# Kernel optimization log

Hardware: AMD Instinct MI355X
Metric: run time of the kernel (lower is better)

Reference implementation:

```python
import jax, jax.numpy as jnp
import numpy as np

NUM_NODES = 10000  # nodes per graph
TOTAL_NODES = 80000  # nbatches (8) * NUM_NODES
N_EDGES = 2560000
IN_DIM, H1, H2 = 128, 32, 64


def setup_inputs() -> dict:
    key = jax.random.key(0)
    ks = jax.random.split(key, 8)
    x = jax.random.normal(ks[0], (TOTAL_NODES, IN_DIM), dtype=jnp.float32)
    ei = jax.random.randint(ks[1], (2, N_EDGES), 0, TOTAL_NODES, dtype=jnp.int64)
    # GCNConv weights (PyG convention: x @ W then propagate, bias after aggregation)
    W1 = jax.random.normal(ks[2], (IN_DIM, H1), dtype=jnp.float32) / np.sqrt(IN_DIM)
    b1 = jax.random.normal(ks[3], (H1,), dtype=jnp.float32) * 0.01
    W2 = jax.random.normal(ks[4], (H1, H2), dtype=jnp.float32) / np.sqrt(H1)
    b2 = jax.random.normal(ks[5], (H2,), dtype=jnp.float32) * 0.01
    Wout = jax.random.normal(ks[6], (H2 * NUM_NODES, 1), dtype=jnp.float32) / np.sqrt(H2 * NUM_NODES)
    bout = jax.random.normal(ks[7], (1,), dtype=jnp.float32) * 0.01
    return {"x": x, "ei": ei, "W1": W1, "b1": b1, "W2": W2, "b2": b2, "Wout": Wout, "bout": bout}


def reference(x, ei, W1, b1, W2, b2, Wout, bout):
    N = x.shape[0]
    # PyG GCNConv: add self-loops, symmetric normalization D^-1/2 (A+I) D^-1/2
    loop = jnp.arange(N, dtype=ei.dtype)
    src = jnp.concatenate([ei[0], loop])
    dst = jnp.concatenate([ei[1], loop])
    deg = jax.ops.segment_sum(jnp.ones_like(src, dtype=x.dtype), dst, num_segments=N)
    dinv = jnp.where(deg > 0, jax.lax.rsqrt(deg), 0.0)
    norm = (dinv[src] * dinv[dst])[:, None]  # [E+N, 1]

    def gcn(h, W, b):
        h = h @ W                     # linear transform first (small feature dim)
        msg = h[src] * norm           # gather + scale
        agg = jax.ops.segment_sum(msg, dst, num_segments=N)  # scatter-add
        return agg + b

    h = jax.nn.relu(gcn(x, W1, b1))
    h = jax.nn.relu(gcn(h, W2, b2))
    nbatches = N // NUM_NODES
    flat = h.reshape(nbatches, NUM_NODES * h.shape[1])
    return flat @ Wout + bout  # [nbatches, 1]
```

## Files before the change

### kernel.cpp

```cpp
#include <hip/hip_runtime.h>
#include <hip/hip_fp16.h>

constexpr int   N_NODES = 80000;
constexpr int   N_EDGE  = 2560000;
constexpr int   IN_DIM  = 128;
constexpr int   H1      = 32;
constexpr int   H2      = 64;
constexpr int   NPB     = 10000;
constexpr int   NB      = 8;
constexpr int   G2_BLOCKS = N_NODES / 8;
constexpr int   BLK_PER_BATCH = G2_BLOCKS / NB;

constexpr int   BKT_SHIFT = 8;
constexpr int   BKT_N     = 1 << BKT_SHIFT;
constexpr int   NBKT      = (N_NODES + BKT_N - 1) >> BKT_SHIFT;
constexpr int   BBSTRIDE  = 16;
constexpr unsigned SBKT_CAP = 9216;
constexpr int   BF_EPB    = 4096;
constexpr int   BF_BLOCKS = N_EDGE / BF_EPB;
constexpr int   BF_THREADS = 512;
constexpr int   BF_EPT    = BF_EPB / BF_THREADS;

constexpr int   G1_ROWS   = 64;
constexpr int   G1_BLOCKS = N_NODES / G1_ROWS;

__global__ void k_initb(unsigned* __restrict__ bbump) {
    int i = blockIdx.x * blockDim.x + threadIdx.x;
    if (i < NBKT) bbump[i * BBSTRIDE] = (unsigned)i * SBKT_CAP;
}

__global__ __launch_bounds__(BF_THREADS) void k_binfill(
        const int* __restrict__ ei, unsigned* __restrict__ bbump,
        unsigned* __restrict__ stage) {
    __shared__ unsigned hist[NBKT];
    __shared__ unsigned base[NBKT];
    int t = threadIdx.x;
    int e0 = blockIdx.x * BF_EPB;
    for (int i = t; i < NBKT; i += BF_THREADS) hist[i] = 0u;
    __syncthreads();
    unsigned dcache[BF_EPT];
#pragma unroll
    for (int k = 0; k < BF_EPT; ++k) {
        unsigned d = (unsigned)ei[N_EDGE + e0 + t + k * BF_THREADS];
        dcache[k] = d;
        atomicAdd(&hist[d >> BKT_SHIFT], 1u);
    }
    __syncthreads();
    for (int i = t; i < NBKT; i += BF_THREADS) {
        unsigned h = hist[i];
        base[i] = h ? atomicAdd(&bbump[i * BBSTRIDE], h) : 0u;
        hist[i] = 0u;
    }
    __syncthreads();
#pragma unroll
    for (int k = 0; k < BF_EPT; ++k) {
        int s = ei[e0 + t + k * BF_THREADS];
        unsigned d = dcache[k];
        int bkt = (int)(d >> BKT_SHIFT);
        unsigned lp = atomicAdd(&hist[bkt], 1u);
        unsigned pos = base[bkt] + lp;
        if (pos < (unsigned)(bkt + 1) * SBKT_CAP)
            stage[pos] = ((unsigned)s << BKT_SHIFT) | (d & (BKT_N - 1u));
    }
}

__global__ __launch_bounds__(256) void k_place(
        const unsigned* __restrict__ bbump, const unsigned* __restrict__ stage,
        int* __restrict__ csr, unsigned* __restrict__ row_ptr,
        unsigned* __restrict__ rend, float* __restrict__ dinv) {
    __shared__ unsigned cnt[BKT_N];
    __shared__ unsigned sc[BKT_N];
    __shared__ unsigned nb[BKT_N];
    int b = blockIdx.x;
    int t = threadIdx.x;
    unsigned beg = (unsigned)b * SBKT_CAP;
    unsigned end = min(bbump[b * BBSTRIDE], (unsigned)(b + 1) * SBKT_CAP);
    cnt[t] = 0u;
    __syncthreads();
    for (unsigned j = beg + (unsigned)t; j < end; j += 256)
        atomicAdd(&cnt[stage[j] & (BKT_N - 1u)], 1u);
    __syncthreads();
    sc[t] = cnt[t];
    for (int ofs = 1; ofs < BKT_N; ofs <<= 1) {
        __syncthreads();
        unsigned u = (t >= ofs) ? sc[t - ofs] : 0u;
        __syncthreads();
        sc[t] += u;
    }
    __syncthreads();
    {
        unsigned nodebase = beg + sc[t] - cnt[t];
        int node = (b << BKT_SHIFT) + t;
        if (node < N_NODES) {
            row_ptr[node] = nodebase;
            rend[node]    = nodebase + cnt[t];
            dinv[node] = rsqrtf((float)(cnt[t] + 1u));
        }
        nb[t] = nodebase;
    }
    __syncthreads();
    for (unsigned j = beg + (unsigned)t; j < end; j += 256) {
        unsigned v = stage[j];
        unsigned pos = atomicAdd(&nb[v & (BKT_N - 1u)], 1u);
        csr[pos] = (int)(v >> BKT_SHIFT);
    }
}

__global__ __launch_bounds__(256) void k_gemm1(
        const float* __restrict__ x, const float* __restrict__ W1,
        const float* __restrict__ dinv, __half* __restrict__ xW1h) {
    __shared__ float W1s[IN_DIM * H1];
    __shared__ float xs[G1_ROWS * IN_DIM];
    int tid = threadIdx.x;
    for (int i = tid; i < IN_DIM * H1; i += 256) W1s[i] = W1[i];
    int row0 = blockIdx.x * G1_ROWS;
    const float4* src4 = reinterpret_cast<const float4*>(x + (size_t)row0 * IN_DIM);
    float4* xs4 = reinterpret_cast<float4*>(xs);
#pragma unroll
    for (int k = 0; k < 8; ++k) xs4[tid + k * 256] = src4[tid + k * 256];
    __syncthreads();
    int c = tid & 31, g = tid >> 5;
    float acc[8] = {0.f, 0.f, 0.f, 0.f, 0.f, 0.f, 0.f, 0.f};
    for (int j = 0; j < IN_DIM / 4; ++j) {
        float w0 = W1s[(4 * j + 0) * H1 + c];
        float w1 = W1s[(4 * j + 1) * H1 + c];
        float w2 = W1s[(4 * j + 2) * H1 + c];
        float w3 = W1s[(4 * j + 3) * H1 + c];
#pragma unroll
        for (int r = 0; r < 8; ++r) {
            float4 a = *reinterpret_cast<const float4*>(&xs[((g * 8 + r) << 7) + 4 * j]);
            acc[r] += a.x * w0 + a.y * w1 + a.z * w2 + a.w * w3;
        }
    }
#pragma unroll
    for (int r = 0; r < 8; ++r) {
        int row = row0 + g * 8 + r;
        xW1h[(size_t)row * H1 + c] = __float2half(acc[r] * dinv[row]);
    }
}

__global__ __launch_bounds__(256) void k_gather1_gemm2(
        const unsigned* __restrict__ row_ptr, const unsigned* __restrict__ rend,
        const int* __restrict__ csr, const __half* __restrict__ xW1h,
        const float* __restrict__ dinv, const float* __restrict__ b1,
        const float* __restrict__ W2, __half* __restrict__ h2h) {
    int wave = threadIdx.x >> 6;
    int lane = threadIdx.x & 63;
    int h = lane >> 5;
    int q = (lane >> 2) & 7;
    int t = lane & 3;
    int d = blockIdx.x * 8 + wave * 2 + h;
    unsigned beg = row_ptr[d], end = rend[d];
    float acc[8] = {0.f, 0.f, 0.f, 0.f, 0.f, 0.f, 0.f, 0.f};
    const __half2 one2  = __float2half2_rn(1.0f);
    const __half2 zero2 = __float2half2_rn(0.0f);
    for (unsigned base = beg; base < end; base += 32) {
        __half2 hacc[4] = {zero2, zero2, zero2, zero2};
#pragma unroll
        for (int it = 0; it < 2; ++it) {
            unsigned j0 = base + (unsigned)(it * 16) + (unsigned)q;
            unsigned j1 = j0 + 8u;
            int     s0 = (j0 < end) ? csr[j0] : 0;
            __half2 m0 = (j0 < end) ? one2 : zero2;
            int     s1 = (j1 < end) ? csr[j1] : 0;
            __half2 m1 = (j1 < end) ? one2 : zero2;
            float4 raw0 = *reinterpret_cast<const float4*>(xW1h + (size_t)s0 * H1 + 8 * t);
            float4 raw1 = *reinterpret_cast<const float4*>(xW1h + (size_t)s1 * H1 + 8 * t);
            const __half2* h0 = reinterpret_cast<const __half2*>(&raw0);
            const __half2* h1 = reinterpret_cast<const __half2*>(&raw1);
#pragma unroll
            for (int i = 0; i < 4; ++i) {
                hacc[i] = __hfma2(h0[i], m0, hacc[i]);
                hacc[i] = __hfma2(h1[i], m1, hacc[i]);
            }
        }
#pragma unroll
        for (int i = 0; i < 4; ++i) {
            float2 f = __half22float2(hacc[i]);
            acc[2 * i]     += f.x;
            acc[2 * i + 1] += f.y;
        }
    }
#pragma unroll
    for (int m = 4; m <= 16; m <<= 1)
#pragma unroll
        for (int i = 0; i < 8; ++i)
            acc[i] += __shfl_xor(acc[i], m, 64);
    float dv = dinv[d];
    float4 sraw = *reinterpret_cast<const float4*>(xW1h + (size_t)d * H1 + 8 * t);
    const __half2* sh = reinterpret_cast<const __half2*>(&sraw);
    float rel[8];
#pragma unroll
    for (int i = 0; i < 4; ++i) {
        float2 f = __half22float2(sh[i]);
        rel[2 * i]     = fmaxf((acc[2 * i]     + f.x) * dv + b1[8 * t + 2 * i],     0.f);
        rel[2 * i + 1] = fmaxf((acc[2 * i + 1] + f.y) * dv + b1[8 * t + 2 * i + 1], 0.f);
    }
    int c = lane & 31;
    float h2a = 0.f, h2b = 0.f;
#pragma unroll
    for (int k = 0; k < H1; ++k) {
        int src = (lane & 32) | (k >> 3);
        float r = __shfl(rel[k & 7], src, 64);
        h2a += r * W2[k * H2 + c];
        h2b += r * W2[k * H2 + c + 32];
    }
    h2h[(size_t)d * H2 + c]      = __float2half(h2a * dv);
    h2h[(size_t)d * H2 + c + 32] = __float2half(h2b * dv);
}

__global__ __launch_bounds__(256) void k_gather2_final(
        const unsigned* __restrict__ row_ptr, const unsigned* __restrict__ rend,
        const int* __restrict__ csr, const __half* __restrict__ h2h,
        const float* __restrict__ dinv, const float* __restrict__ b2,
        const float* __restrict__ Wout, double* __restrict__ partial2) {
    int wave = threadIdx.x >> 6;
    int lane = threadIdx.x & 63;
    int h = lane >> 5;
    int o = (lane >> 3) & 3;
    int t = lane & 7;
    int d = blockIdx.x * 8 + wave * 2 + h;
    unsigned beg = row_ptr[d], end = rend[d];
    float acc[8] = {0.f, 0.f, 0.f, 0.f, 0.f, 0.f, 0.f, 0.f};
    const __half2 one2  = __float2half2_rn(1.0f);
    const __half2 zero2 = __float2half2_rn(0.0f);
    for (unsigned base = beg; base < end; base += 16) {
        __half2 hacc[4] = {zero2, zero2, zero2, zero2};
#pragma unroll
        for (int it = 0; it < 2; ++it) {
            unsigned j0 = base + (unsigned)(it * 8) + (unsigned)o;
            unsigned j1 = j0 + 4u;
            int     s0 = (j0 < end) ? csr[j0] : 0;
            __half2 m0 = (j0 < end) ? one2 : zero2;
            int     s1 = (j1 < end) ? csr[j1] : 0;
            __half2 m1 = (j1 < end) ? one2 : zero2;
            float4 raw0 = *reinterpret_cast<const float4*>(h2h + (size_t)s0 * H2 + 8 * t);
            float4 raw1 = *reinterpret_cast<const float4*>(h2h + (size_t)s1 * H2 + 8 * t);
            const __half2* h0 = reinterpret_cast<const __half2*>(&raw0);
            const __half2* h1 = reinterpret_cast<const __half2*>(&raw1);
#pragma unroll
            for (int i = 0; i < 4; ++i) {
                hacc[i] = __hfma2(h0[i], m0, hacc[i]);
                hacc[i] = __hfma2(h1[i], m1, hacc[i]);
            }
        }
#pragma unroll
        for (int i = 0; i < 4; ++i) {
            float2 f = __half22float2(hacc[i]);
            acc[2 * i]     += f.x;
            acc[2 * i + 1] += f.y;
        }
    }
#pragma unroll
    for (int m = 8; m <= 16; m <<= 1)
#pragma unroll
        for (int i = 0; i < 8; ++i)
            acc[i] += __shfl_xor(acc[i], m, 64);
    float dv = dinv[d];
    float4 sraw = *reinterpret_cast<const float4*>(h2h + (size_t)d * H2 + 8 * t);
    const __half2* sh = reinterpret_cast<const __half2*>(&sraw);
    float4 bb0 = *reinterpret_cast<const float4*>(b2 + 8 * t);
    float4 bb1 = *reinterpret_cast<const float4*>(b2 + 8 * t + 4);
    const float* wrow = Wout + (size_t)(d % NPB) * H2 + 8 * t;
    float4 ww0 = *reinterpret_cast<const float4*>(wrow);
    float4 ww1 = *reinterpret_cast<const float4*>(wrow + 4);
    float self[8];
#pragma unroll
    for (int i = 0; i < 4; ++i) {
        float2 f = __half22float2(sh[i]);
        self[2 * i] = f.x; self[2 * i + 1] = f.y;
    }
    float bbv[8] = {bb0.x, bb0.y, bb0.z, bb0.w, bb1.x, bb1.y, bb1.z, bb1.w};
    float wwv[8] = {ww0.x, ww0.y, ww0.z, ww0.w, ww1.x, ww1.y, ww1.z, ww1.w};
    float fsum = 0.f;
#pragma unroll
    for (int i = 0; i < 8; ++i)
        fsum += fmaxf((acc[i] + self[i]) * dv + bbv[i], 0.f) * wwv[i];
    double dval = (double)fsum;
    dval += __shfl_down(dval, 4, 64);
    dval += __shfl_down(dval, 2, 64);
    dval += __shfl_down(dval, 1, 64);
    __shared__ double sdbl[8];
    if ((lane & 31) == 0) sdbl[wave * 2 + h] = dval;
    __syncthreads();
    if (threadIdx.x == 0)
        partial2[blockIdx.x] = ((sdbl[0] + sdbl[1]) + (sdbl[2] + sdbl[3]))
                             + ((sdbl[4] + sdbl[5]) + (sdbl[6] + sdbl[7]));
}

__global__ __launch_bounds__(256) void k_reduce(
        const double* __restrict__ partial2, const float* __restrict__ bout,
        float* __restrict__ out) {
    int b = blockIdx.x;
    int tid = threadIdx.x;
    double acc = 0.0;
    for (int i = tid; i < BLK_PER_BATCH; i += 256)
        acc += partial2[b * BLK_PER_BATCH + i];
    for (int off = 32; off; off >>= 1) acc += __shfl_down(acc, off, 64);
    __shared__ double sred[4];
    if ((tid & 63) == 0) sred[tid >> 6] = acc;
    __syncthreads();
    if (tid == 0)
        out[b] = (float)(((sred[0] + sred[1]) + (sred[2] + sred[3])) + (double)bout[0]);
}

extern "C" void kernel_launch(void* const* d_in, const int* in_sizes, int n_in,
                              void* d_out, int out_size, void* d_ws, size_t ws_size,
                              hipStream_t stream) {
    const float* x    = (const float*)d_in[0];
    const int*   ei   = (const int*)d_in[1];
    const float* W1   = (const float*)d_in[2];
    const float* b1   = (const float*)d_in[3];
    const float* W2   = (const float*)d_in[4];
    const float* b2   = (const float*)d_in[5];
    const float* Wout = (const float*)d_in[6];
    const float* bout = (const float*)d_in[7];
    float* out = (float*)d_out;

    constexpr size_t STATIC_SZ = (size_t)NBKT * SBKT_CAP;
    char* ws = (char*)d_ws;
    size_t off = 0;
    int*      csr     = (int*)(ws + off);      off += STATIC_SZ * 4;
    unsigned* stage   = (unsigned*)(ws + off); off += STATIC_SZ * 4;
    __half*   xW1h    = (__half*)(ws + off);   off += (size_t)N_NODES * H1 * 2;
    __half*   h2h     = (__half*)(ws + off);   off += (size_t)N_NODES * H2 * 2;
    unsigned* row_ptr = (unsigned*)(ws + off); off += (size_t)N_NODES * 4;
    unsigned* rend    = (unsigned*)(ws + off); off += (size_t)N_NODES * 4;
    float*    dinv    = (float*)(ws + off);    off += (size_t)N_NODES * 4;
    unsigned* bbump   = (unsigned*)(ws + off); off += (size_t)NBKT * BBSTRIDE * 4;
    double*   partial2= (double*)(ws + off);   off += (size_t)G2_BLOCKS * 8;
    (void)ws_size; (void)in_sizes; (void)n_in; (void)out_size;

    const int B = 256;
    k_initb<<<(NBKT + B - 1) / B, B, 0, stream>>>(bbump);
    k_binfill<<<BF_BLOCKS, BF_THREADS, 0, stream>>>(ei, bbump, stage);
    k_place<<<NBKT, B, 0, stream>>>(bbump, stage, csr, row_ptr, rend, dinv);

    k_gemm1<<<G1_BLOCKS, B, 0, stream>>>(x, W1, dinv, xW1h);
    k_gather1_gemm2<<<N_NODES / 8, B, 0, stream>>>(row_ptr, rend, csr, xW1h, dinv, b1, W2, h2h);
    k_gather2_final<<<G2_BLOCKS, B, 0, stream>>>(row_ptr, rend, csr, h2h, dinv, b2, Wout, partial2);

    k_reduce<<<NB, B, 0, stream>>>(partial2, bout, out);
}
```

Measured before the change: 175.0 us.

## Merge GEMM1 into edge binning launch and apply dinv scaling in place

The first-layer GEMM no longer depends on dinv, so it now runs as extra blocks of the edge-binning kernel. This overlaps the compute-heavy GEMM with the atomic-heavy binning and saves one launch. The per-node dinv scaling of xW1 moves into k_place, which rescales its bucket's fp16 rows in place. The cost is an extra read-modify-write pass over xW1h and a second fp16 rounding. The fused kernel also uses a 48KB static shared buffer, which can lower occupancy for the binning blocks.

```diff
diff --git a/kernel.cpp b/kernel.cpp
--- a/kernel.cpp
+++ b/kernel.cpp
@@ -18,59 +18,96 @@
 constexpr unsigned SBKT_CAP = 9216;
 constexpr int   BF_EPB    = 4096;
 constexpr int   BF_BLOCKS = N_EDGE / BF_EPB;
-constexpr int   BF_THREADS = 512;
-constexpr int   BF_EPT    = BF_EPB / BF_THREADS;
+constexpr int   FB_THREADS = 512;
+constexpr int   BF_EPT    = BF_EPB / FB_THREADS;
 
 constexpr int   G1_ROWS   = 64;
 constexpr int   G1_BLOCKS = N_NODES / G1_ROWS;
+constexpr int   FUSED_BLOCKS = BF_BLOCKS + G1_BLOCKS;
 
 __global__ void k_initb(unsigned* __restrict__ bbump) {
     int i = blockIdx.x * blockDim.x + threadIdx.x;
     if (i < NBKT) bbump[i * BBSTRIDE] = (unsigned)i * SBKT_CAP;
 }
 
-__global__ __launch_bounds__(BF_THREADS) void k_binfill(
+__global__ __launch_bounds__(FB_THREADS) void k_binfill_gemm1(
         const int* __restrict__ ei, unsigned* __restrict__ bbump,
-        unsigned* __restrict__ stage) {
-    __shared__ unsigned hist[NBKT];
-    __shared__ unsigned base[NBKT];
+        unsigned* __restrict__ stage,
+        const float* __restrict__ x, const float* __restrict__ W1,
+        __half* __restrict__ xW1h) {
+    __shared__ __align__(16) char smem[49152];
     int t = threadIdx.x;
-    int e0 = blockIdx.x * BF_EPB;
-    for (int i = t; i < NBKT; i += BF_THREADS) hist[i] = 0u;
-    __syncthreads();
-    unsigned dcache[BF_EPT];
-#pragma unroll
-    for (int k = 0; k < BF_EPT; ++k) {
-        unsigned d = (unsigned)ei[N_EDGE + e0 + t + k * BF_THREADS];
-        dcache[k] = d;
-        atomicAdd(&hist[d >> BKT_SHIFT], 1u);
-    }
-    __syncthreads();
-    for (int i = t; i < NBKT; i += BF_THREADS) {
-        unsigned h = hist[i];
-        base[i] = h ? atomicAdd(&bbump[i * BBSTRIDE], h) : 0u;
-        hist[i] = 0u;
-    }
-    __syncthreads();
-#pragma unroll
-    for (int k = 0; k < BF_EPT; ++k) {
-        int s = ei[e0 + t + k * BF_THREADS];
-        unsigned d = dcache[k];
-        int bkt = (int)(d >> BKT_SHIFT);
-        unsigned lp = atomicAdd(&hist[bkt], 1u);
-        unsigned pos = base[bkt] + lp;
-        if (pos < (unsigned)(bkt + 1) * SBKT_CAP)
-            stage[pos] = ((unsigned)s << BKT_SHIFT) | (d & (BKT_N - 1u));
+    if (blockIdx.x < BF_BLOCKS) {
+        unsigned* hist = (unsigned*)smem;
+        unsigned* base = hist + NBKT;
+        int e0 = blockIdx.x * BF_EPB;
+        for (int i = t; i < NBKT; i += FB_THREADS) hist[i] = 0u;
+        __syncthreads();
+        unsigned dcache[BF_EPT];
+#pragma unroll
+        for (int k = 0; k < BF_EPT; ++k) {
+            unsigned d = (unsigned)ei[N_EDGE + e0 + t + k * FB_THREADS];
+            dcache[k] = d;
+            atomicAdd(&hist[d >> BKT_SHIFT], 1u);
+        }
+        __syncthreads();
+        for (int i = t; i < NBKT; i += FB_THREADS) {
+            unsigned h = hist[i];
+            base[i] = h ? atomicAdd(&bbump[i * BBSTRIDE], h) : 0u;
+            hist[i] = 0u;
+        }
+        __syncthreads();
+#pragma unroll
+        for (int k = 0; k < BF_EPT; ++k) {
+            int s = ei[e0 + t + k * FB_THREADS];
+            unsigned d = dcache[k];
+            int bkt = (int)(d >> BKT_SHIFT);
+            unsigned lp = atomicAdd(&hist[bkt], 1u);
+            unsigned pos = base[bkt] + lp;
+            if (pos < (unsigned)(bkt + 1) * SBKT_CAP)
+                stage[pos] = ((unsigned)s << BKT_SHIFT) | (d & (BKT_N - 1u));
+        }
+    } else {
+        float* W1s = (float*)smem;
+        float* xs  = W1s + IN_DIM * H1;
+        int bb = blockIdx.x - BF_BLOCKS;
+        int row0 = bb * G1_ROWS;
+        for (int i = t; i < IN_DIM * H1; i += FB_THREADS) W1s[i] = W1[i];
+        const float4* src4 = reinterpret_cast<const float4*>(x + (size_t)row0 * IN_DIM);
+        float4* xs4 = reinterpret_cast<float4*>(xs);
+#pragma unroll
+        for (int k = 0; k < 4; ++k) xs4[t + k * FB_THREADS] = src4[t + k * FB_THREADS];
+        __syncthreads();
+        int c = t & 31, g = t >> 5;
+        float acc[4] = {0.f, 0.f, 0.f, 0.f};
+        for (int j = 0; j < IN_DIM / 4; ++j) {
+            float w0 = W1s[(4 * j + 0) * H1 + c];
+            float w1 = W1s[(4 * j + 1) * H1 + c];
+            float w2 = W1s[(4 * j + 2) * H1 + c];
+            float w3 = W1s[(4 * j + 3) * H1 + c];
+#pragma unroll
+            for (int r = 0; r < 4; ++r) {
+                float4 a = *reinterpret_cast<const float4*>(&xs[((g * 4 + r) << 7) + 4 * j]);
+                acc[r] += a.x * w0 + a.y * w1 + a.z * w2 + a.w * w3;
+            }
+        }
+#pragma unroll
+        for (int r = 0; r < 4; ++r) {
+            int row = row0 + g * 4 + r;
+            xW1h[(size_t)row * H1 + c] = __float2half(acc[r]);
+        }
     }
 }
 
 __global__ __launch_bounds__(256) void k_place(
         const unsigned* __restrict__ bbump, const unsigned* __restrict__ stage,
         int* __restrict__ csr, unsigned* __restrict__ row_ptr,
-        unsigned* __restrict__ rend, float* __restrict__ dinv) {
+        unsigned* __restrict__ rend, float* __restrict__ dinv,
+        __half* __restrict__ xW1h) {
     __shared__ unsigned cnt[BKT_N];
     __shared__ unsigned sc[BKT_N];
     __shared__ unsigned nb[BKT_N];
+    __shared__ float    dvs[BKT_N];
     int b = blockIdx.x;
     int t = threadIdx.x;
     unsigned beg = (unsigned)b * SBKT_CAP;
@@ -89,14 +126,16 @@
     }
     __syncthreads();
     {
+        float dvloc = rsqrtf((float)(cnt[t] + 1u));
         unsigned nodebase = beg + sc[t] - cnt[t];
         int node = (b << BKT_SHIFT) + t;
         if (node < N_NODES) {
             row_ptr[node] = nodebase;
             rend[node]    = nodebase + cnt[t];
-            dinv[node] = rsqrtf((float)(cnt[t] + 1u));
+            dinv[node] = dvloc;
         }
         nb[t] = nodebase;
+        dvs[t] = dvloc;
     }
     __syncthreads();
     for (unsigned j = beg + (unsigned)t; j < end; j += 256) {
@@ -104,38 +143,13 @@
         unsigned pos = atomicAdd(&nb[v & (BKT_N - 1u)], 1u);
         csr[pos] = (int)(v >> BKT_SHIFT);
     }
-}
-
-__global__ __launch_bounds__(256) void k_gemm1(
-        const float* __restrict__ x, const float* __restrict__ W1,
-        const float* __restrict__ dinv, __half* __restrict__ xW1h) {
-    __shared__ float W1s[IN_DIM * H1];
-    __shared__ float xs[G1_ROWS * IN_DIM];
-    int tid = threadIdx.x;
-    for (int i = tid; i < IN_DIM * H1; i += 256) W1s[i] = W1[i];
-    int row0 = blockIdx.x * G1_ROWS;
-    const float4* src4 = reinterpret_cast<const float4*>(x + (size_t)row0 * IN_DIM);
-    float4* xs4 = reinterpret_cast<float4*>(xs);
-#pragma unroll
-    for (int k = 0; k < 8; ++k) xs4[tid + k * 256] = src4[tid + k * 256];
-    __syncthreads();
-    int c = tid & 31, g = tid >> 5;
-    float acc[8] = {0.f, 0.f, 0.f, 0.f, 0.f, 0.f, 0.f, 0.f};
-    for (int j = 0; j < IN_DIM / 4; ++j) {
-        float w0 = W1s[(4 * j + 0) * H1 + c];
-        float w1 = W1s[(4 * j + 1) * H1 + c];
-        float w2 = W1s[(4 * j + 2) * H1 + c];
-        float w3 = W1s[(4 * j + 3) * H1 + c];
-#pragma unroll
-        for (int r = 0; r < 8; ++r) {
-            float4 a = *reinterpret_cast<const float4*>(&xs[((g * 8 + r) << 7) + 4 * j]);
-            acc[r] += a.x * w0 + a.y * w1 + a.z * w2 + a.w * w3;
-        }
-    }
-#pragma unroll
-    for (int r = 0; r < 8; ++r) {
-        int row = row0 + g * 8 + r;
-        xW1h[(size_t)row * H1 + c] = __float2half(acc[r] * dinv[row]);
+    int n0 = b << BKT_SHIFT;
+    int nvalid = min(BKT_N, N_NODES - n0);
+    __half2* rows = reinterpret_cast<__half2*>(xW1h + (size_t)n0 * H1);
+    for (int idx = t; idx < nvalid * (H1 / 2); idx += 256) {
+        float dv = dvs[idx >> 4];
+        float2 f = __half22float2(rows[idx]);
+        rows[idx] = __floats2half2_rn(f.x * dv, f.y * dv);
     }
 }
 
@@ -333,10 +347,9 @@
 
     const int B = 256;
     k_initb<<<(NBKT + B - 1) / B, B, 0, stream>>>(bbump);
-    k_binfill<<<BF_BLOCKS, BF_THREADS, 0, stream>>>(ei, bbump, stage);
-    k_place<<<NBKT, B, 0, stream>>>(bbump, stage, csr, row_ptr, rend, dinv);
-
-    k_gemm1<<<G1_BLOCKS, B, 0, stream>>>(x, W1, dinv, xW1h);
+    k_binfill_gemm1<<<FUSED_BLOCKS, FB_THREADS, 0, stream>>>(ei, bbump, stage, x, W1, xW1h);
+    k_place<<<NBKT, B, 0, stream>>>(bbump, stage, csr, row_ptr, rend, dinv, xW1h);
+
     k_gather1_gemm2<<<N_NODES / 8, B, 0, stream>>>(row_ptr, rend, csr, xW1h, dinv, b1, W2, h2h);
     k_gather2_final<<<G2_BLOCKS, B, 0, stream>>>(row_ptr, rend, csr, h2h, dinv, b2, Wout, partial2);
 
```

New measurement: 169.6 us, median of 2. -3.1%, faster.
